# Performance work log

Hardware: AMD Instinct MI355X
Metric: run time of the kernel (lower is better)

Reference implementation:

```python
import jax, jax.numpy as jnp
import numpy as np

B, N, D = 4, 4096, 1024
DFF = 4 * D
K = 2048  # max(1, int(N * 0.5))


def setup_inputs() -> dict:
    key = jax.random.key(0)
    ks = jax.random.split(key, 4)
    x = jax.random.normal(ks[0], (B, N, D), dtype=jnp.float32)
    gate_w = jax.random.normal(ks[1], (1, D), dtype=jnp.float32) * 0.02
    w1 = jax.random.normal(ks[2], (D, DFF), dtype=jnp.float32) * (1.0 / np.sqrt(D))
    b1 = jnp.zeros((DFF,), dtype=jnp.float32)
    w2 = jax.random.normal(ks[3], (DFF, D), dtype=jnp.float32) * (1.0 / np.sqrt(DFF))
    b2 = jnp.zeros((D,), dtype=jnp.float32)
    return {"x": x, "gate_w": gate_w, "w1": w1, "b1": b1, "w2": w2, "b2": b2, "k": K}


def reference(x, gate_w, w1, b1, w2, b2, k):
    # scores: [B, N] = gate(x).squeeze(-1)
    scores = jnp.einsum("bnd,d->bn", x, gate_w[0])
    _, topk = jax.lax.top_k(scores, k)          # [B, k] token indices
    # gather selected tokens: [B, k, D]
    x_sel = jnp.take_along_axis(x, topk[:, :, None], axis=1)
    # ffn (d -> 4d -> d, GELU) + residual on selected tokens only
    h = jax.nn.gelu(x_sel @ w1 + b1) @ w2 + b2
    x_proc = x_sel + h
    # scatter processed tokens back into a copy of x
    b_idx = jnp.arange(x.shape[0])[:, None]      # [B, 1]
    out = x.at[b_idx, topk].set(x_proc)
    return out
```

## Files before the change

### kernel.cpp

```cpp
#include <hip/hip_runtime.h>
#include <math.h>

#define B_   4
#define N_   4096
#define D_   1024
#define DFF_ 4096
#define K_   2048

typedef __attribute__((ext_vector_type(8))) short short8;
typedef __attribute__((ext_vector_type(4))) float float4v;

__device__ __forceinline__ unsigned short f2bf(float f) {
    unsigned int u = __float_as_uint(f);
    u = (u + 0x7fffu + ((u >> 16) & 1u)) >> 16;
    return (unsigned short)u;
}

__device__ __forceinline__ void gld16(const void* g, void* l) {
    __builtin_amdgcn_global_load_lds((const __attribute__((address_space(1))) void*)g,
                                     (__attribute__((address_space(3))) void*)l, 16, 0, 0);
}

__global__ __launch_bounds__(256) void scores_kernel(const float* __restrict__ x,
                                                     const float* __restrict__ gate_w,
                                                     float* __restrict__ scores,
                                                     int* __restrict__ slot) {
    int wave = (blockIdx.x * blockDim.x + threadIdx.x) >> 6;
    int lane = threadIdx.x & 63;
    if (wave >= B_ * N_) return;
    if (lane == 1) slot[wave] = -1;
    const float4* xr = (const float4*)(x + (size_t)wave * D_);
    const float4* g  = (const float4*)gate_w;
    float acc = 0.f;
    #pragma unroll
    for (int j = 0; j < D_ / 4 / 64; ++j) {
        float4 a = xr[lane + j * 64];
        float4 b = g[lane + j * 64];
        acc += a.x * b.x + a.y * b.y + a.z * b.z + a.w * b.w;
    }
    #pragma unroll
    for (int off = 32; off > 0; off >>= 1) acc += __shfl_down(acc, off, 64);
    if (lane == 0) scores[wave] = acc;
}

__global__ __launch_bounds__(1024) void select_topk_kernel(const float* __restrict__ scores,
                                                           int* __restrict__ topk,
                                                           int* __restrict__ slot) {
    __shared__ unsigned key[N_];
    __shared__ unsigned hist[256];
    __shared__ int sh_bin, sh_rem, sh_ngt;
    __shared__ int wsum[16], woff[16];
    int b = blockIdx.x, tid = threadIdx.x;
    int lane = tid & 63, wid = tid >> 6;

    for (int i = tid; i < N_; i += 1024) {
        unsigned u = __float_as_uint(scores[b * N_ + i]);
        key[i] = (u & 0x80000000u) ? ~u : (u | 0x80000000u);
    }
    if (tid == 0) sh_ngt = 0;
    __syncthreads();

    unsigned prefix = 0, pmask = 0;
    int rem = K_;
    for (int shift = 24; shift >= 0; shift -= 8) {
        if (tid < 256) hist[tid] = 0;
        __syncthreads();
        for (int i = tid; i < N_; i += 1024) {
            unsigned k = key[i];
            if ((k & pmask) == prefix) atomicAdd(&hist[(k >> shift) & 255u], 1u);
        }
        __syncthreads();
        if (tid < 64) {
            unsigned v0 = hist[4 * lane], v1 = hist[4 * lane + 1];
            unsigned v2 = hist[4 * lane + 2], v3 = hist[4 * lane + 3];
            unsigned s3 = v3, s2 = v2 + s3, s1 = v1 + s2, s0 = v0 + s1;
            unsigned t = s0;
            #pragma unroll
            for (int off = 1; off < 64; off <<= 1) {
                unsigned u = __shfl_down(t, off, 64);
                if (lane + off < 64) t += u;
            }
            unsigned above = t - s0;
            unsigned S0 = s0 + above, S1 = s1 + above, S2 = s2 + above, S3 = s3 + above;
            unsigned R = (unsigned)rem;
            if (S0 >= R && S1 < R) { sh_bin = 4 * lane;     sh_rem = rem - (int)S1; }
            if (S1 >= R && S2 < R) { sh_bin = 4 * lane + 1; sh_rem = rem - (int)S2; }
            if (S2 >= R && S3 < R) { sh_bin = 4 * lane + 2; sh_rem = rem - (int)S3; }
            if (S3 >= R && above < R) { sh_bin = 4 * lane + 3; sh_rem = rem - (int)above; }
        }
        __syncthreads();
        prefix |= ((unsigned)sh_bin) << shift;
        pmask  |= 0xffu << shift;
        rem = sh_rem;
    }
    unsigned T = prefix;
    int c_gt = K_ - rem;

    for (int i = tid; i < N_; i += 1024) {
        bool p = key[i] > T;
        unsigned long long m = __ballot(p);
        int cnt = __popcll(m);
        int basepos = 0;
        if (lane == 0 && cnt) basepos = atomicAdd(&sh_ngt, cnt);
        basepos = __shfl(basepos, 0, 64);
        if (p) {
            int pos = basepos + __popcll(m & ((1ULL << lane) - 1ULL));
            topk[b * K_ + pos] = i;
            slot[b * N_ + i] = b * K_ + pos;
        }
    }
    int base = tid * 4, c = 0;
    #pragma unroll
    for (int j = 0; j < 4; ++j) c += (key[base + j] == T);
    int sc = c;
    #pragma unroll
    for (int off = 1; off < 64; off <<= 1) {
        int u = __shfl_up(sc, off, 64);
        if (lane >= off) sc += u;
    }
    if (lane == 63) wsum[wid] = sc;
    __syncthreads();
    if (tid == 0) {
        int run = 0;
        #pragma unroll
        for (int j = 0; j < 16; ++j) { woff[j] = run; run += wsum[j]; }
    }
    __syncthreads();
    int r = woff[wid] + sc - c;
    #pragma unroll
    for (int j = 0; j < 4; ++j) {
        if (key[base + j] == T) {
            if (r < rem) {
                topk[b * K_ + c_gt + r] = base + j;
                slot[b * N_ + base + j] = b * K_ + c_gt + r;
            }
            ++r;
        }
    }
}

__global__ __launch_bounds__(256) void gather_copy_kernel(const float* __restrict__ x,
                                                          const int* __restrict__ slot,
                                                          unsigned short* __restrict__ xsel,
                                                          float* __restrict__ out) {
    int row = blockIdx.x;
    int t = threadIdx.x;
    int s = slot[row];
    float4 v = ((const float4*)(x + (size_t)row * D_))[t];
    if (s >= 0) {
        ushort4 o;
        o.x = f2bf(v.x); o.y = f2bf(v.y); o.z = f2bf(v.z); o.w = f2bf(v.w);
        ((ushort4*)(xsel + (size_t)s * D_))[t] = o;
    } else {
        ((float4*)(out + (size_t)row * D_))[t] = v;
    }
}

__global__ __launch_bounds__(256) void transpose_both_kernel(const float* __restrict__ w1,
                                                             const float* __restrict__ w2,
                                                             unsigned short* __restrict__ w1t,
                                                             unsigned short* __restrict__ w2t) {
    __shared__ float tile[32][33];
    int bid = blockIdx.x;
    const float* src; unsigned short* dst; int R, C, bx, by;
    if (bid < 4096) { src = w1; dst = w1t; R = D_;   C = DFF_; bx = bid & 127;          by = bid >> 7; }
    else            { src = w2; dst = w2t; R = DFF_; C = D_;   bx = (bid - 4096) & 31;  by = (bid - 4096) >> 5; }
    int tx = threadIdx.x & 31, ty = threadIdx.x >> 5;
    int c = bx * 32 + tx, r0 = by * 32;
    #pragma unroll
    for (int j = ty; j < 32; j += 8) tile[j][tx] = src[(size_t)(r0 + j) * C + c];
    __syncthreads();
    int dc = by * 32 + tx, dr0 = bx * 32;
    #pragma unroll
    for (int j = ty; j < 32; j += 8) dst[(size_t)(dr0 + j) * R + dc] = f2bf(tile[tx][j]);
}

__global__ __launch_bounds__(256) void ffn1_mfma_kernel(const unsigned short* __restrict__ A,
                                                        const unsigned short* __restrict__ Bt,
                                                        const float* __restrict__ b1,
                                                        unsigned short* __restrict__ h1) {
    constexpr int K = D_;
    __shared__ __align__(16) unsigned short smem[16384];
    unsigned short* As = smem;
    unsigned short* Bs = smem + 4096;
    unsigned short* Cs = smem;
    int t = threadIdx.x;
    int w = t >> 6, lane = t & 63;
    int quad = lane >> 4, lr = lane & 15;
    int wm = w >> 1, wn = w & 1;
    int row0 = blockIdx.x * 128, col0 = blockIdx.y * 128;

    const char* ga0 = (const char*)(A + (size_t)(row0 + (t >> 2)) * K) + (t & 3) * 16;
    const char* ga1 = ga0 + (size_t)64 * K * 2;
    const char* gb0 = (const char*)(Bt + (size_t)(col0 + (t >> 2)) * K) + (t & 3) * 16;
    const char* gb1 = gb0 + (size_t)64 * K * 2;
    unsigned short* la0 = As + t * 8;   unsigned short* la1 = As + 2048 + t * 8;
    unsigned short* lb0 = Bs + t * 8;   unsigned short* lb1 = Bs + 2048 + t * 8;

    float4v acc[4][4] = {};
    for (int k0 = 0; k0 < K; k0 += 32) {
        gld16(ga0, la0); gld16(ga1, la1);
        gld16(gb0, lb0); gld16(gb1, lb1);
        ga0 += 64; ga1 += 64; gb0 += 64; gb1 += 64;
        __syncthreads();
        short8 af[4], bfv[4];
        #pragma unroll
        for (int mi = 0; mi < 4; ++mi)
            af[mi] = *(const short8*)(As + (size_t)(wm * 64 + mi * 16 + lr) * 32 + quad * 8);
        #pragma unroll
        for (int ni = 0; ni < 4; ++ni)
            bfv[ni] = *(const short8*)(Bs + (size_t)(wn * 64 + ni * 16 + lr) * 32 + quad * 8);
        #pragma unroll
        for (int mi = 0; mi < 4; ++mi)
            #pragma unroll
            for (int ni = 0; ni < 4; ++ni)
                acc[mi][ni] = __builtin_amdgcn_mfma_f32_16x16x32_bf16(af[mi], bfv[ni], acc[mi][ni], 0, 0, 0);
        __syncthreads();
    }

    #pragma unroll
    for (int half = 0; half < 2; ++half) {
        __syncthreads();
        #pragma unroll
        for (int mi2 = 0; mi2 < 2; ++mi2) {
            int mi = half * 2 + mi2;
            #pragma unroll
            for (int ni = 0; ni < 4; ++ni) {
                int col = wn * 64 + ni * 16 + lr;
                float bias = b1[col0 + col];
                #pragma unroll
                for (int r = 0; r < 4; ++r) {
                    int lrow = wm * 32 + mi2 * 16 + quad * 4 + r;
                    float u = acc[mi][ni][r] + bias;
                    float tt = 1.5957691216057308f * u * (1.0f + 0.044715f * u * u);
                    float g = u / (1.0f + __expf(-tt));
                    Cs[lrow * 132 + col] = f2bf(g);
                }
            }
        }
        __syncthreads();
        #pragma unroll
        for (int kch = 0; kch < 4; ++kch) {
            int ch = t + kch * 256;
            int lrow = ch >> 4;
            int off = (ch & 15) * 8;
            int grow = row0 + ((lrow >> 5) << 6) + half * 32 + (lrow & 31);
            *(short8*)(h1 + (size_t)grow * DFF_ + col0 + off) = *(const short8*)(Cs + lrow * 132 + off);
        }
    }
}

__global__ __launch_bounds__(256) void ffn2_mfma_kernel(const unsigned short* __restrict__ A,
                                                        const unsigned short* __restrict__ Bt,
                                                        const float* __restrict__ b2,
                                                        const float* __restrict__ x,
                                                        const int* __restrict__ topk,
                                                        float* __restrict__ out) {
    constexpr int K = DFF_;
    __shared__ __align__(16) unsigned short As[128 * 32];
    __shared__ __align__(16) unsigned short Bs[128 * 32];
    int t = threadIdx.x;
    int w = t >> 6, lane = t & 63;
    int quad = lane >> 4, lr = lane & 15;
    int wm = w >> 1, wn = w & 1;
    int row0 = blockIdx.x * 128, col0 = blockIdx.y * 128;

    const char* ga0 = (const char*)(A + (size_t)(row0 + (t >> 2)) * K) + (t & 3) * 16;
    const char* ga1 = ga0 + (size_t)64 * K * 2;
    const char* gb0 = (const char*)(Bt + (size_t)(col0 + (t >> 2)) * K) + (t & 3) * 16;
    const char* gb1 = gb0 + (size_t)64 * K * 2;
    unsigned short* la0 = As + t * 8;   unsigned short* la1 = As + 2048 + t * 8;
    unsigned short* lb0 = Bs + t * 8;   unsigned short* lb1 = Bs + 2048 + t * 8;

    float4v acc[4][4] = {};
    for (int k0 = 0; k0 < K; k0 += 32) {
        gld16(ga0, la0); gld16(ga1, la1);
        gld16(gb0, lb0); gld16(gb1, lb1);
        ga0 += 64; ga1 += 64; gb0 += 64; gb1 += 64;
        __syncthreads();
        short8 af[4], bfv[4];
        #pragma unroll
        for (int mi = 0; mi < 4; ++mi)
            af[mi] = *(const short8*)(As + (size_t)(wm * 64 + mi * 16 + lr) * 32 + quad * 8);
        #pragma unroll
        for (int ni = 0; ni < 4; ++ni)
            bfv[ni] = *(const short8*)(Bs + (size_t)(wn * 64 + ni * 16 + lr) * 32 + quad * 8);
        #pragma unroll
        for (int mi = 0; mi < 4; ++mi)
            #pragma unroll
            for (int ni = 0; ni < 4; ++ni)
                acc[mi][ni] = __builtin_amdgcn_mfma_f32_16x16x32_bf16(af[mi], bfv[ni], acc[mi][ni], 0, 0, 0);
        __syncthreads();
    }

    #pragma unroll
    for (int mi = 0; mi < 4; ++mi) {
        #pragma unroll
        for (int r = 0; r < 4; ++r) {
            int row = row0 + wm * 64 + mi * 16 + quad * 4 + r;
            int gb = row >> 11;
            int tok = topk[row];
            size_t base = ((size_t)(gb * N_ + tok)) * D_;
            #pragma unroll
            for (int ni = 0; ni < 4; ++ni) {
                int col = col0 + wn * 64 + ni * 16 + lr;
                out[base + col] = x[base + col] + acc[mi][ni][r] + b2[col];
            }
        }
    }
}

extern "C" void kernel_launch(void* const* d_in, const int* in_sizes, int n_in,
                              void* d_out, int out_size, void* d_ws, size_t ws_size,
                              hipStream_t stream) {
    const float* x      = (const float*)d_in[0];
    const float* gate_w = (const float*)d_in[1];
    const float* w1     = (const float*)d_in[2];
    const float* b1     = (const float*)d_in[3];
    const float* w2     = (const float*)d_in[4];
    const float* b2     = (const float*)d_in[5];
    float* out = (float*)d_out;

    char* ws = (char*)d_ws;
    float*          scores = (float*)ws;
    int*            topk   = (int*)(ws + (64 << 10));
    int*            slot   = (int*)(ws + (96 << 10));
    unsigned short* xsel   = (unsigned short*)(ws + (160 << 10));
    unsigned short* w1t    = (unsigned short*)(ws + (160 << 10) + (16 << 20));
    unsigned short* w2t    = (unsigned short*)(ws + (160 << 10) + (24 << 20));
    unsigned short* h1     = (unsigned short*)(ws + (160 << 10) + (32 << 20));

    scores_kernel<<<(B_ * N_) / 4, 256, 0, stream>>>(x, gate_w, scores, slot);
    select_topk_kernel<<<B_, 1024, 0, stream>>>(scores, topk, slot);

    transpose_both_kernel<<<8192, 256, 0, stream>>>(w1, w2, w1t, w2t);

    gather_copy_kernel<<<B_ * N_, 256, 0, stream>>>(x, slot, xsel, out);

    ffn1_mfma_kernel<<<dim3(64, 32), 256, 0, stream>>>(xsel, w1t, b1, h1);
    ffn2_mfma_kernel<<<dim3(64, 8), 256, 0, stream>>>(h1, w2t, b2, x, topk, out);
}
```

Measured before the change: 352.1 us.

## Merge scores and weight-transpose kernels; stage ffn2 epilogue through LDS for vector stores

The gate-score computation and the bf16 transpose of w1/w2 now run in one launch, so the launch gap between them goes away and the memory-bound scoring can overlap with the transposes. The ffn2 epilogue writes each accumulator tile to shared memory in 32-row chunks and then does coalesced float4 reads of x and float4 writes to the scattered output rows. Previously these were strided scalar accesses. The shared buffers are enlarged to hold the staging tile, and the epilogue adds extra barriers.

Result: no change. 358.8 us (+1.9%).

```diff
diff --git a/kernel.cpp b/kernel.cpp
--- a/kernel.cpp
+++ b/kernel.cpp
@@ -21,26 +21,46 @@
                                      (__attribute__((address_space(3))) void*)l, 16, 0, 0);
 }
 
-__global__ __launch_bounds__(256) void scores_kernel(const float* __restrict__ x,
-                                                     const float* __restrict__ gate_w,
-                                                     float* __restrict__ scores,
-                                                     int* __restrict__ slot) {
-    int wave = (blockIdx.x * blockDim.x + threadIdx.x) >> 6;
-    int lane = threadIdx.x & 63;
-    if (wave >= B_ * N_) return;
-    if (lane == 1) slot[wave] = -1;
-    const float4* xr = (const float4*)(x + (size_t)wave * D_);
-    const float4* g  = (const float4*)gate_w;
-    float acc = 0.f;
-    #pragma unroll
-    for (int j = 0; j < D_ / 4 / 64; ++j) {
-        float4 a = xr[lane + j * 64];
-        float4 b = g[lane + j * 64];
-        acc += a.x * b.x + a.y * b.y + a.z * b.z + a.w * b.w;
-    }
-    #pragma unroll
-    for (int off = 32; off > 0; off >>= 1) acc += __shfl_down(acc, off, 64);
-    if (lane == 0) scores[wave] = acc;
+__global__ __launch_bounds__(256) void scores_transpose_kernel(const float* __restrict__ x,
+                                                               const float* __restrict__ gate_w,
+                                                               float* __restrict__ scores,
+                                                               int* __restrict__ slot,
+                                                               const float* __restrict__ w1,
+                                                               const float* __restrict__ w2,
+                                                               unsigned short* __restrict__ w1t,
+                                                               unsigned short* __restrict__ w2t) {
+    __shared__ float tile[32][33];
+    int bid = blockIdx.x;
+    if (bid < 4096) {
+        int wave = (bid * 256 + threadIdx.x) >> 6;
+        int lane = threadIdx.x & 63;
+        if (lane == 1) slot[wave] = -1;
+        const float4* xr = (const float4*)(x + (size_t)wave * D_);
+        const float4* g  = (const float4*)gate_w;
+        float acc = 0.f;
+        #pragma unroll
+        for (int j = 0; j < D_ / 4 / 64; ++j) {
+            float4 a = xr[lane + j * 64];
+            float4 b = g[lane + j * 64];
+            acc += a.x * b.x + a.y * b.y + a.z * b.z + a.w * b.w;
+        }
+        #pragma unroll
+        for (int off = 32; off > 0; off >>= 1) acc += __shfl_down(acc, off, 64);
+        if (lane == 0) scores[wave] = acc;
+        return;
+    }
+    int tb = bid - 4096;
+    const float* src; unsigned short* dst; int R, C, bx, by;
+    if (tb < 4096) { src = w1; dst = w1t; R = D_;   C = DFF_; bx = tb & 127;          by = tb >> 7; }
+    else           { src = w2; dst = w2t; R = DFF_; C = D_;   bx = (tb - 4096) & 31;  by = (tb - 4096) >> 5; }
+    int tx = threadIdx.x & 31, ty = threadIdx.x >> 5;
+    int c = bx * 32 + tx, r0 = by * 32;
+    #pragma unroll
+    for (int j = ty; j < 32; j += 8) tile[j][tx] = src[(size_t)(r0 + j) * C + c];
+    __syncthreads();
+    int dc = by * 32 + tx, dr0 = bx * 32;
+    #pragma unroll
+    for (int j = ty; j < 32; j += 8) dst[(size_t)(dr0 + j) * R + dc] = f2bf(tile[tx][j]);
 }
 
 __global__ __launch_bounds__(1024) void select_topk_kernel(const float* __restrict__ scores,
@@ -156,34 +176,15 @@
     }
 }
 
-__global__ __launch_bounds__(256) void transpose_both_kernel(const float* __restrict__ w1,
-                                                             const float* __restrict__ w2,
-                                                             unsigned short* __restrict__ w1t,
-                                                             unsigned short* __restrict__ w2t) {
-    __shared__ float tile[32][33];
-    int bid = blockIdx.x;
-    const float* src; unsigned short* dst; int R, C, bx, by;
-    if (bid < 4096) { src = w1; dst = w1t; R = D_;   C = DFF_; bx = bid & 127;          by = bid >> 7; }
-    else            { src = w2; dst = w2t; R = DFF_; C = D_;   bx = (bid - 4096) & 31;  by = (bid - 4096) >> 5; }
-    int tx = threadIdx.x & 31, ty = threadIdx.x >> 5;
-    int c = bx * 32 + tx, r0 = by * 32;
-    #pragma unroll
-    for (int j = ty; j < 32; j += 8) tile[j][tx] = src[(size_t)(r0 + j) * C + c];
-    __syncthreads();
-    int dc = by * 32 + tx, dr0 = bx * 32;
-    #pragma unroll
-    for (int j = ty; j < 32; j += 8) dst[(size_t)(dr0 + j) * R + dc] = f2bf(tile[tx][j]);
-}
-
 __global__ __launch_bounds__(256) void ffn1_mfma_kernel(const unsigned short* __restrict__ A,
                                                         const unsigned short* __restrict__ Bt,
                                                         const float* __restrict__ b1,
                                                         unsigned short* __restrict__ h1) {
     constexpr int K = D_;
-    __shared__ __align__(16) unsigned short smem[16384];
-    unsigned short* As = smem;
-    unsigned short* Bs = smem + 4096;
-    unsigned short* Cs = smem;
+    __shared__ __align__(16) char smem[16896];
+    unsigned short* As = (unsigned short*)smem;
+    unsigned short* Bs = As + 4096;
+    unsigned short* Cs = (unsigned short*)smem;
     int t = threadIdx.x;
     int w = t >> 6, lane = t & 63;
     int quad = lane >> 4, lr = lane & 15;
@@ -257,8 +258,10 @@
                                                         const int* __restrict__ topk,
                                                         float* __restrict__ out) {
     constexpr int K = DFF_;
-    __shared__ __align__(16) unsigned short As[128 * 32];
-    __shared__ __align__(16) unsigned short Bs[128 * 32];
+    __shared__ __align__(16) char smem[16896];
+    unsigned short* As = (unsigned short*)smem;
+    unsigned short* Bs = As + 4096;
+    float* Cs = (float*)smem;
     int t = threadIdx.x;
     int w = t >> 6, lane = t & 63;
     int quad = lane >> 4, lr = lane & 15;
@@ -294,18 +297,40 @@
     }
 
     #pragma unroll
-    for (int mi = 0; mi < 4; ++mi) {
-        #pragma unroll
-        for (int r = 0; r < 4; ++r) {
-            int row = row0 + wm * 64 + mi * 16 + quad * 4 + r;
-            int gb = row >> 11;
-            int tok = topk[row];
-            size_t base = ((size_t)(gb * N_ + tok)) * D_;
-            #pragma unroll
-            for (int ni = 0; ni < 4; ++ni) {
-                int col = col0 + wn * 64 + ni * 16 + lr;
-                out[base + col] = x[base + col] + acc[mi][ni][r] + b2[col];
+    for (int q = 0; q < 4; ++q) {
+        __syncthreads();
+        if (wm == (q >> 1)) {
+            #pragma unroll
+            for (int mi2 = 0; mi2 < 2; ++mi2) {
+                int mi = (q & 1) * 2 + mi2;
+                #pragma unroll
+                for (int ni = 0; ni < 4; ++ni) {
+                    int col = wn * 64 + ni * 16 + lr;
+                    #pragma unroll
+                    for (int r = 0; r < 4; ++r)
+                        Cs[(mi2 * 16 + quad * 4 + r) * 132 + col] = acc[mi][ni][r];
+                }
             }
+        }
+        __syncthreads();
+        #pragma unroll
+        for (int kch = 0; kch < 4; ++kch) {
+            int ch = t + kch * 256;
+            int lrow = ch >> 5;
+            int c4 = (ch & 31) * 4;
+            int grow = row0 + q * 32 + lrow;
+            int gb = grow >> 11;
+            int tok = topk[grow];
+            size_t base = ((size_t)(gb * N_ + tok)) * D_ + col0 + c4;
+            float4 xv = *(const float4*)(x + base);
+            float4 bv = *(const float4*)(b2 + col0 + c4);
+            const float* cp = Cs + lrow * 132 + c4;
+            float4 o;
+            o.x = xv.x + cp[0] + bv.x;
+            o.y = xv.y + cp[1] + bv.y;
+            o.z = xv.z + cp[2] + bv.z;
+            o.w = xv.w + cp[3] + bv.w;
+            *(float4*)(out + base) = o;
         }
     }
 }
@@ -330,11 +355,8 @@
     unsigned short* w2t    = (unsigned short*)(ws + (160 << 10) + (24 << 20));
     unsigned short* h1     = (unsigned short*)(ws + (160 << 10) + (32 << 20));
 
-    scores_kernel<<<(B_ * N_) / 4, 256, 0, stream>>>(x, gate_w, scores, slot);
+    scores_transpose_kernel<<<12288, 256, 0, stream>>>(x, gate_w, scores, slot, w1, w2, w1t, w2t);
     select_topk_kernel<<<B_, 1024, 0, stream>>>(scores, topk, slot);
-
-    transpose_both_kernel<<<8192, 256, 0, stream>>>(w1, w2, w1t, w2t);
-
     gather_copy_kernel<<<B_ * N_, 256, 0, stream>>>(x, slot, xsel, out);
 
     ffn1_mfma_kernel<<<dim3(64, 32), 256, 0, stream>>>(xsel, w1t, b1, h1);
```
